# Kernel tuning notes

Measured on AMD Instinct MI355X. Metric: run time of the kernel, lower is better.

## Reference

```python
import jax, jax.numpy as jnp
import numpy as np

B, S, HID = 2, 2048, 2816
NH, NKV, HD = 16, 8, 256
WINDOW = 1024
EPS = 1e-6
ROPE_THETA = 10000.0


def _rope_cos_sin(batch, seq, dim, theta):
    inv_freq = 1.0 / (theta ** (np.arange(0, dim, 2, dtype=np.float32) / dim))  # [dim/2]
    pos = np.arange(seq, dtype=np.float32)
    freqs = np.outer(pos, inv_freq)                 # [S, dim/2]
    emb = np.concatenate([freqs, freqs], axis=-1)   # [S, dim]
    cos = np.broadcast_to(np.cos(emb), (batch, seq, dim))
    sin = np.broadcast_to(np.sin(emb), (batch, seq, dim))
    return jnp.asarray(cos), jnp.asarray(sin)


def setup_inputs() -> dict:
    key = jax.random.key(0)
    ks = jax.random.split(key, 6)
    hidden_states = jax.random.normal(ks[0], (B, S, HID), dtype=jnp.float32)
    sc = 0.02
    Wq = jax.random.normal(ks[1], (NH * HD, HID), dtype=jnp.float32) * sc
    Wk = jax.random.normal(ks[2], (NKV * HD, HID), dtype=jnp.float32) * sc
    Wv = jax.random.normal(ks[3], (NKV * HD, HID), dtype=jnp.float32) * sc
    Wo = jax.random.normal(ks[4], (HID, NH * HD), dtype=jnp.float32) * sc
    q_norm_w = jnp.ones((HD,), dtype=jnp.float32) + 0.1 * jax.random.normal(ks[5], (HD,), dtype=jnp.float32)
    k_norm_w = jnp.ones((HD,), dtype=jnp.float32)
    cos, sin = _rope_cos_sin(B, S, HD, ROPE_THETA)
    return {"hidden_states": hidden_states, "Wq": Wq, "Wk": Wk, "Wv": Wv,
            "Wo": Wo, "q_norm_w": q_norm_w, "k_norm_w": k_norm_w,
            "cos": cos, "sin": sin}


def _rmsnorm(x, w):
    # HF Gemma4: effective weight, no +1 offset
    var = jnp.mean(jnp.square(x), axis=-1, keepdims=True)
    return x * jax.lax.rsqrt(var + EPS) * w


def _rotate_half(x):
    h = x.shape[-1] // 2
    return jnp.concatenate([-x[..., h:], x[..., :h]], axis=-1)


def reference(hidden_states, Wq, Wk, Wv, Wo, q_norm_w, k_norm_w, cos, sin):
    b, s, _ = hidden_states.shape
    q = (hidden_states @ Wq.T).reshape(b, s, NH, HD)
    k = (hidden_states @ Wk.T).reshape(b, s, NKV, HD)
    v = (hidden_states @ Wv.T).reshape(b, s, NKV, HD)
    q = _rmsnorm(q, q_norm_w)
    k = _rmsnorm(k, k_norm_w)
    v = _rmsnorm(v, jnp.ones((HD,), dtype=v.dtype))  # v_norm has no scale
    # RoPE with explicit cos/sin, unsqueeze at head dim (2)
    c = cos[:, :, None, :]
    sn = sin[:, :, None, :]
    q = q * c + _rotate_half(q) * sn
    k = k * c + _rotate_half(k) * sn
    # GQA: repeat kv heads to match query heads
    rep = NH // NKV
    k = jnp.repeat(k, rep, axis=2)  # [b,s,NH,HD]
    v = jnp.repeat(v, rep, axis=2)
    # scale=1.0 per torch_attention call (no 1/sqrt(d))
    scores = jnp.einsum('bqhd,bkhd->bhqk', q, k)
    i = jnp.arange(s)[:, None]
    j = jnp.arange(s)[None, :]
    mask = (j <= i) & (i - j < WINDOW)  # causal + sliding window
    scores = jnp.where(mask[None, None], scores, jnp.finfo(scores.dtype).min)
    attn = jax.nn.softmax(scores, axis=-1)
    out = jnp.einsum('bhqk,bkhd->bqhd', attn, v)  # [b,s,NH,HD]
    return out.reshape(b, s, NH * HD) @ Wo.T
```

## Files before the change

### kernel.cpp

```cpp
#include <hip/hip_runtime.h>
#include <math.h>

typedef unsigned short u16;
typedef __attribute__((ext_vector_type(8))) short short8;
typedef __attribute__((ext_vector_type(8))) _Float16 half8;
typedef __attribute__((ext_vector_type(4))) float floatx4;

#define NH 16
#define NKV 8
#define HD 256
#define SEQ 2048
#define BATCH 2
#define QD (NH * HD)
#define KVD (NKV * HD)
#define TOKS (BATCH * SEQ)
#define WINDOW 1024

__device__ __forceinline__ u16 f2h(float f) {
    _Float16 h = (_Float16)f;
    return __builtin_bit_cast(u16, h);
}
__device__ __forceinline__ float h2f(u16 u) {
    return (float)__builtin_bit_cast(_Float16, u);
}

__device__ __forceinline__ void gload16(const u16* g, u16* l) {
    __builtin_amdgcn_global_load_lds(
        (const __attribute__((address_space(1))) unsigned int*)g,
        (__attribute__((address_space(3))) unsigned int*)l,
        16, 0, 0);
}

__global__ __launch_bounds__(256) void f32_to_f16(const float* __restrict__ in,
                                                  u16* __restrict__ out, int n8) {
    const int i = blockIdx.x * 256 + threadIdx.x;
    if (i >= n8) return;
    const float4 a = *((const float4*)in + 2 * (size_t)i);
    const float4 b = *((const float4*)in + 2 * (size_t)i + 1);
    short8 r;
    r[0] = (short)f2h(a.x); r[1] = (short)f2h(a.y);
    r[2] = (short)f2h(a.z); r[3] = (short)f2h(a.w);
    r[4] = (short)f2h(b.x); r[5] = (short)f2h(b.y);
    r[6] = (short)f2h(b.z); r[7] = (short)f2h(b.w);
    *((short8*)out + i) = r;
}

template<bool OUTF32, bool OUTT>
__global__ __launch_bounds__(256) void gemm_lds(const u16* __restrict__ A,
                                                const u16* __restrict__ B,
                                                void* __restrict__ Cp,
                                                int M, int N, int K) {
    __shared__ u16 As[128 * 32];
    __shared__ u16 Bs[128 * 32];

    const int tid = threadIdx.x;
    const int wave = tid >> 6, lane = tid & 63;
    const int quad = lane >> 4, l16 = lane & 15;
    const int bm = blockIdx.y * 128, bn = blockIdx.x * 128;
    const int wm = (wave >> 1) * 64, wn = (wave & 1) * 64;

    const int srow = wave * 32 + (lane >> 2);
    const int scol = (lane & 3) * 8;
    const u16* ga0 = A + (size_t)(bm + srow) * K + scol;
    const u16* ga1 = ga0 + (size_t)16 * K;
    const u16* gb0 = B + (size_t)(bn + srow) * K + scol;
    const u16* gb1 = gb0 + (size_t)16 * K;
    u16* lA0 = &As[wave * 1024];
    u16* lA1 = &As[wave * 1024 + 512];
    u16* lB0 = &Bs[wave * 1024];
    u16* lB1 = &Bs[wave * 1024 + 512];

    floatx4 acc[4][4];
#pragma unroll
    for (int i = 0; i < 4; ++i)
#pragma unroll
        for (int j = 0; j < 4; ++j) acc[i][j] = (floatx4){0.f, 0.f, 0.f, 0.f};

    const int kTiles = K >> 5;
    for (int kt = 0; kt < kTiles; ++kt) {
        __syncthreads();
        gload16(ga0, lA0);
        gload16(ga1, lA1);
        gload16(gb0, lB0);
        gload16(gb1, lB1);
        ga0 += 32; ga1 += 32; gb0 += 32; gb1 += 32;
        __syncthreads();

        half8 af[4], bfr[4];
#pragma unroll
        for (int i = 0; i < 4; ++i)
            af[i] = *(const half8*)(&As[(wm + i * 16 + l16) * 32 + quad * 8]);
#pragma unroll
        for (int j = 0; j < 4; ++j)
            bfr[j] = *(const half8*)(&Bs[(wn + j * 16 + l16) * 32 + quad * 8]);
#pragma unroll
        for (int i = 0; i < 4; ++i)
#pragma unroll
            for (int j = 0; j < 4; ++j)
                acc[i][j] = __builtin_amdgcn_mfma_f32_16x16x32_f16(af[i], bfr[j], acc[i][j], 0, 0, 0);
    }

#pragma unroll
    for (int i = 0; i < 4; ++i) {
#pragma unroll
        for (int j = 0; j < 4; ++j) {
            const int row0 = bm + wm + i * 16 + quad * 4;
            const int col = bn + wn + j * 16 + l16;
#pragma unroll
            for (int r = 0; r < 4; ++r) {
                if constexpr (OUTT)
                    ((u16*)Cp)[(size_t)col * M + row0 + r] = f2h(acc[i][j][r]);
                else if constexpr (OUTF32)
                    ((float*)Cp)[(size_t)(row0 + r) * N + col] = acc[i][j][r];
                else
                    ((u16*)Cp)[(size_t)(row0 + r) * N + col] = f2h(acc[i][j][r]);
            }
        }
    }
}

__global__ __launch_bounds__(256) void norm_rope_kernel(
        u16* __restrict__ Q, u16* __restrict__ K,
        const float* __restrict__ qw, const float* __restrict__ kw,
        const float* __restrict__ cosp, const float* __restrict__ sinp) {
    const int w = blockIdx.x * 4 + (threadIdx.x >> 6);
    const int lane = threadIdx.x & 63;
    const int row = w >> 5;
    const int sub = w & 31;
    if (sub >= 24) return;

    u16* ptr;
    const float* wt;
    if (sub < 16) { ptr = Q + (size_t)row * QD + sub * HD;         wt = qw; }
    else          { ptr = K + (size_t)row * KVD + (sub - 16) * HD; wt = kw; }

    const int d = lane * 4;
    uint2 raw = *(const uint2*)(ptr + d);
    float x[4];
    x[0] = h2f((u16)(raw.x & 0xffffu));
    x[1] = h2f((u16)(raw.x >> 16));
    x[2] = h2f((u16)(raw.y & 0xffffu));
    x[3] = h2f((u16)(raw.y >> 16));

    float ss = x[0] * x[0] + x[1] * x[1] + x[2] * x[2] + x[3] * x[3];
#pragma unroll
    for (int m = 1; m < 64; m <<= 1) ss += __shfl_xor(ss, m, 64);
    const float sc = rsqrtf(ss * (1.0f / 256.0f) + 1e-6f);

    float nrm[4];
#pragma unroll
    for (int i = 0; i < 4; ++i) nrm[i] = x[i] * sc * wt[d + i];

    const size_t cbase = (size_t)row * HD + d;
    const float sgn = (lane < 32) ? -1.0f : 1.0f;
    float out[4];
#pragma unroll
    for (int i = 0; i < 4; ++i) {
        float pn = __shfl_xor(nrm[i], 32, 64);
        float c = cosp[cbase + i];
        float s = sinp[cbase + i];
        out[i] = nrm[i] * c + sgn * pn * s;
    }

    uint2 o;
    o.x = (unsigned int)f2h(out[0]) | ((unsigned int)f2h(out[1]) << 16);
    o.y = (unsigned int)f2h(out[2]) | ((unsigned int)f2h(out[3]) << 16);
    *(uint2*)(ptr + d) = o;
}

__global__ __launch_bounds__(256) void vnorm_kernel(u16* __restrict__ Vt) {
    const int tok = blockIdx.x * 256 + threadIdx.x;
    const int kvh = blockIdx.y;
    u16* p = Vt + (size_t)kvh * HD * TOKS + tok;
    float ss = 0.f;
#pragma unroll 4
    for (int d = 0; d < HD; ++d) {
        float v = h2f(p[(size_t)d * TOKS]);
        ss += v * v;
    }
    const float sc = rsqrtf(ss * (1.0f / 256.0f) + 1e-6f);
#pragma unroll 4
    for (int d = 0; d < HD; ++d) {
        const size_t idx = (size_t)d * TOKS;
        p[idx] = f2h(h2f(p[idx]) * sc);
    }
}

#define QBLK 64
#define KVBLK 64

__global__ __launch_bounds__(256, 2) void attn_mfma(
        const u16* __restrict__ Q, const u16* __restrict__ K,
        const u16* __restrict__ Vt, u16* __restrict__ O) {
    __shared__ u16 Ks[64 * 264];
    __shared__ u16 Vs[256 * 72];
    __shared__ u16 Ps[4][16 * 72];

    const int tid = threadIdx.x;
    const int wave = tid >> 6, lane = tid & 63;
    const int quad = lane >> 4, l16 = lane & 15;
    const int q0 = blockIdx.x * QBLK;
    const int h = blockIdx.y, b = blockIdx.z;
    const int kvh = h >> 1;

    half8 qf[8];
    {
        const u16* qp = Q + (size_t)(b * SEQ + q0 + wave * 16 + l16) * QD + h * HD + quad * 8;
#pragma unroll
        for (int s = 0; s < 8; ++s) qf[s] = *(const half8*)(qp + s * 32);
    }

    float mrow[4], lrow[4];
#pragma unroll
    for (int r = 0; r < 4; ++r) { mrow[r] = -1e30f; lrow[r] = 0.f; }
    floatx4 o[16];
#pragma unroll
    for (int n = 0; n < 16; ++n) o[n] = (floatx4){0.f, 0.f, 0.f, 0.f};

    int lo = q0 - (WINDOW - 1);
    const int t0 = (lo > 0 ? lo : 0) >> 6;
    const int tq = q0 >> 6;

    for (int t = t0; t <= tq; ++t) {
        const int k0 = t * KVBLK;
        __syncthreads();
        {
            const int r = tid >> 5, c = (tid & 31) * 8;
            const u16* kp = K + (size_t)(b * SEQ + k0 + r) * KVD + kvh * HD + c;
#pragma unroll
            for (int p = 0; p < 8; ++p)
                *(short8*)(&Ks[(r + p * 8) * 264 + c]) = *(const short8*)(kp + (size_t)(p * 8) * KVD);
        }
        {
            const int r = tid >> 3, c = (tid & 7) * 8;
            const u16* vp = Vt + (size_t)(kvh * HD + r) * TOKS + b * SEQ + k0 + c;
#pragma unroll
            for (int p = 0; p < 8; ++p)
                *(short8*)(&Vs[(r + p * 32) * 72 + c]) = *(const short8*)(vp + (size_t)(p * 32) * TOKS);
        }
        __syncthreads();

        floatx4 sf[4];
#pragma unroll
        for (int j = 0; j < 4; ++j) sf[j] = (floatx4){0.f, 0.f, 0.f, 0.f};
#pragma unroll
        for (int s = 0; s < 8; ++s) {
#pragma unroll
            for (int j = 0; j < 4; ++j) {
                half8 bf = *(const half8*)(&Ks[(j * 16 + l16) * 264 + s * 32 + quad * 8]);
                sf[j] = __builtin_amdgcn_mfma_f32_16x16x32_f16(qf[s], bf, sf[j], 0, 0, 0);
            }
        }

        const bool needMask = (t == tq) || ((q0 + QBLK - 1) - k0 >= WINDOW);
        if (needMask) {
#pragma unroll
            for (int j = 0; j < 4; ++j) {
                const int kg = k0 + j * 16 + l16;
#pragma unroll
                for (int r = 0; r < 4; ++r) {
                    const int qg = q0 + wave * 16 + quad * 4 + r;
                    if (kg > qg || qg - kg >= WINDOW) sf[j][r] = -1e30f;
                }
            }
        }

#pragma unroll
        for (int r = 0; r < 4; ++r) {
            float mx = fmaxf(fmaxf(sf[0][r], sf[1][r]), fmaxf(sf[2][r], sf[3][r]));
            mx = fmaxf(mx, __shfl_xor(mx, 1, 64));
            mx = fmaxf(mx, __shfl_xor(mx, 2, 64));
            mx = fmaxf(mx, __shfl_xor(mx, 4, 64));
            mx = fmaxf(mx, __shfl_xor(mx, 8, 64));
            const float mnew = fmaxf(mrow[r], mx);
            const float rescale = __expf(mrow[r] - mnew);
            mrow[r] = mnew;
            float pv[4], ssum = 0.f;
#pragma unroll
            for (int j = 0; j < 4; ++j) {
                pv[j] = __expf(sf[j][r] - mnew);
                ssum += pv[j];
            }
            ssum += __shfl_xor(ssum, 1, 64);
            ssum += __shfl_xor(ssum, 2, 64);
            ssum += __shfl_xor(ssum, 4, 64);
            ssum += __shfl_xor(ssum, 8, 64);
            lrow[r] = lrow[r] * rescale + ssum;
#pragma unroll
            for (int n = 0; n < 16; ++n) o[n][r] *= rescale;
#pragma unroll
            for (int j = 0; j < 4; ++j)
                Ps[wave][(quad * 4 + r) * 72 + j * 16 + l16] = f2h(pv[j]);
        }

#pragma unroll
        for (int s2 = 0; s2 < 2; ++s2) {
            half8 pa = *(const half8*)(&Ps[wave][l16 * 72 + s2 * 32 + quad * 8]);
#pragma unroll
            for (int n = 0; n < 16; ++n) {
                half8 vb = *(const half8*)(&Vs[(n * 16 + l16) * 72 + s2 * 32 + quad * 8]);
                o[n] = __builtin_amdgcn_mfma_f32_16x16x32_f16(pa, vb, o[n], 0, 0, 0);
            }
        }
    }

#pragma unroll
    for (int r = 0; r < 4; ++r) {
        const float inv = 1.0f / lrow[r];
        const size_t base = (size_t)(b * SEQ + q0 + wave * 16 + quad * 4 + r) * QD + h * HD + l16;
#pragma unroll
        for (int n = 0; n < 16; ++n)
            O[base + n * 16] = f2h(o[n][r] * inv);
    }
}

extern "C" void kernel_launch(void* const* d_in, const int* in_sizes, int n_in,
                              void* d_out, int out_size, void* d_ws, size_t ws_size,
                              hipStream_t stream) {
    const float* X    = (const float*)d_in[0];
    const float* Wq   = (const float*)d_in[1];
    const float* Wk   = (const float*)d_in[2];
    const float* Wv   = (const float*)d_in[3];
    const float* Wo   = (const float*)d_in[4];
    const float* qw   = (const float*)d_in[5];
    const float* kw   = (const float*)d_in[6];
    const float* cosp = (const float*)d_in[7];
    const float* sinp = (const float*)d_in[8];

    char* ws = (char*)d_ws;
    u16* Qb  = (u16*)(ws);
    u16* Kb  = (u16*)(ws + (size_t)33554432);
    u16* Vt  = (u16*)(ws + (size_t)50331648);
    u16* Ob  = (u16*)(ws + (size_t)67108864);
    u16* Wkh = (u16*)(ws + (size_t)67108864);
    u16* Wvh = (u16*)(ws + (size_t)78643200);
    u16* Woh = (u16*)(ws);

    u16* Xh  = (u16*)d_out;
    u16* Wqh = (u16*)d_out + (size_t)11534336;

    const dim3 blk(256);
    f32_to_f16<<<dim3(5632), blk, 0, stream>>>(X,  Xh,  11534336 / 8);
    f32_to_f16<<<dim3(5632), blk, 0, stream>>>(Wq, Wqh, 11534336 / 8);
    gemm_lds<false, false><<<dim3(4096 / 128, 4096 / 128), blk, 0, stream>>>(Xh, Wqh, Qb, 4096, 4096, 2816);
    f32_to_f16<<<dim3(2816), blk, 0, stream>>>(Wk, Wkh, 5767168 / 8);
    gemm_lds<false, false><<<dim3(2048 / 128, 4096 / 128), blk, 0, stream>>>(Xh, Wkh, Kb, 4096, 2048, 2816);
    f32_to_f16<<<dim3(2816), blk, 0, stream>>>(Wv, Wvh, 5767168 / 8);
    gemm_lds<false, true ><<<dim3(2048 / 128, 4096 / 128), blk, 0, stream>>>(Xh, Wvh, Vt, 4096, 2048, 2816);
    norm_rope_kernel<<<dim3((BATCH * SEQ * 32) / 4), blk, 0, stream>>>(Qb, Kb, qw, kw, cosp, sinp);
    vnorm_kernel<<<dim3(TOKS / 256, NKV), blk, 0, stream>>>(Vt);
    attn_mfma<<<dim3(SEQ / QBLK, NH, BATCH), blk, 0, stream>>>(Qb, Kb, Vt, Ob);
    f32_to_f16<<<dim3(5632), blk, 0, stream>>>(Wo, Woh, 11534336 / 8);
    gemm_lds<true, false><<<dim3(2816 / 128, 4096 / 128), blk, 0, stream>>>(Ob, Woh, d_out, 4096, 2816, 4096);
}
```

Measured before the change: 858.4 us.

## Fuse QKV projections into one GEMM and swizzle attention LDS with async loads

The three Q/K/V projection GEMMs become one launch over a concatenated fp16 weight matrix. Each output tile is routed to Q, K or transposed V storage depending on its column block. The attention kernel now loads its K/V tiles with direct global-to-LDS 16-byte loads into unpadded, XOR-swizzled shared buffers, replacing register-staged copies into padded arrays. It also raises wave priority around the MFMA sections. The intent is fewer launches, better GEMM occupancy, less LDS footprint and fewer bank conflicts, at the cost of more complex addressing and fp16 buffers placed in the output region.

Result: faster. 833.3 us (-2.9%).

```diff
diff --git a/kernel.cpp b/kernel.cpp
--- a/kernel.cpp
+++ b/kernel.cpp
@@ -45,61 +45,58 @@
     *((short8*)out + i) = r;
 }
 
-template<bool OUTF32, bool OUTT>
+#define GEMM_PRE()                                                            \
+    __shared__ u16 As[128 * 32];                                              \
+    __shared__ u16 Bs[128 * 32];                                              \
+    const int tid = threadIdx.x;                                              \
+    const int wave = tid >> 6, lane = tid & 63;                               \
+    const int quad = lane >> 4, l16 = lane & 15;                              \
+    const int bm = blockIdx.y * 128, bn = blockIdx.x * 128;                   \
+    const int wm = (wave >> 1) * 64, wn = (wave & 1) * 64;                    \
+    const int srow = wave * 32 + (lane >> 2);                                 \
+    const int scol = (lane & 3) * 8;                                          \
+    const u16* ga0 = A + (size_t)(bm + srow) * K + scol;                      \
+    const u16* ga1 = ga0 + (size_t)16 * K;                                    \
+    const u16* gb0 = B + (size_t)(bn + srow) * K + scol;                      \
+    const u16* gb1 = gb0 + (size_t)16 * K;                                    \
+    u16* lA0 = &As[wave * 1024];                                              \
+    u16* lA1 = &As[wave * 1024 + 512];                                        \
+    u16* lB0 = &Bs[wave * 1024];                                              \
+    u16* lB1 = &Bs[wave * 1024 + 512];                                        \
+    floatx4 acc[4][4];                                                        \
+    _Pragma("unroll")                                                         \
+    for (int i = 0; i < 4; ++i)                                               \
+        _Pragma("unroll")                                                     \
+        for (int j = 0; j < 4; ++j) acc[i][j] = (floatx4){0.f, 0.f, 0.f, 0.f};\
+    const int kTiles = K >> 5;                                                \
+    for (int kt = 0; kt < kTiles; ++kt) {                                     \
+        __syncthreads();                                                      \
+        gload16(ga0, lA0);                                                    \
+        gload16(ga1, lA1);                                                    \
+        gload16(gb0, lB0);                                                    \
+        gload16(gb1, lB1);                                                    \
+        ga0 += 32; ga1 += 32; gb0 += 32; gb1 += 32;                           \
+        __syncthreads();                                                      \
+        half8 af[4], bfr[4];                                                  \
+        _Pragma("unroll")                                                     \
+        for (int i = 0; i < 4; ++i)                                           \
+            af[i] = *(const half8*)(&As[(wm + i * 16 + l16) * 32 + quad * 8]);\
+        _Pragma("unroll")                                                     \
+        for (int j = 0; j < 4; ++j)                                           \
+            bfr[j] = *(const half8*)(&Bs[(wn + j * 16 + l16) * 32 + quad * 8]);\
+        _Pragma("unroll")                                                     \
+        for (int i = 0; i < 4; ++i)                                           \
+            _Pragma("unroll")                                                 \
+            for (int j = 0; j < 4; ++j)                                       \
+                acc[i][j] = __builtin_amdgcn_mfma_f32_16x16x32_f16(af[i], bfr[j], acc[i][j], 0, 0, 0); \
+    }
+
+template<bool OUTF32>
 __global__ __launch_bounds__(256) void gemm_lds(const u16* __restrict__ A,
                                                 const u16* __restrict__ B,
                                                 void* __restrict__ Cp,
                                                 int M, int N, int K) {
-    __shared__ u16 As[128 * 32];
-    __shared__ u16 Bs[128 * 32];
-
-    const int tid = threadIdx.x;
-    const int wave = tid >> 6, lane = tid & 63;
-    const int quad = lane >> 4, l16 = lane & 15;
-    const int bm = blockIdx.y * 128, bn = blockIdx.x * 128;
-    const int wm = (wave >> 1) * 64, wn = (wave & 1) * 64;
-
-    const int srow = wave * 32 + (lane >> 2);
-    const int scol = (lane & 3) * 8;
-    const u16* ga0 = A + (size_t)(bm + srow) * K + scol;
-    const u16* ga1 = ga0 + (size_t)16 * K;
-    const u16* gb0 = B + (size_t)(bn + srow) * K + scol;
-    const u16* gb1 = gb0 + (size_t)16 * K;
-    u16* lA0 = &As[wave * 1024];
-    u16* lA1 = &As[wave * 1024 + 512];
-    u16* lB0 = &Bs[wave * 1024];
-    u16* lB1 = &Bs[wave * 1024 + 512];
-
-    floatx4 acc[4][4];
-#pragma unroll
-    for (int i = 0; i < 4; ++i)
-#pragma unroll
-        for (int j = 0; j < 4; ++j) acc[i][j] = (floatx4){0.f, 0.f, 0.f, 0.f};
-
-    const int kTiles = K >> 5;
-    for (int kt = 0; kt < kTiles; ++kt) {
-        __syncthreads();
-        gload16(ga0, lA0);
-        gload16(ga1, lA1);
-        gload16(gb0, lB0);
-        gload16(gb1, lB1);
-        ga0 += 32; ga1 += 32; gb0 += 32; gb1 += 32;
-        __syncthreads();
-
-        half8 af[4], bfr[4];
-#pragma unroll
-        for (int i = 0; i < 4; ++i)
-            af[i] = *(const half8*)(&As[(wm + i * 16 + l16) * 32 + quad * 8]);
-#pragma unroll
-        for (int j = 0; j < 4; ++j)
-            bfr[j] = *(const half8*)(&Bs[(wn + j * 16 + l16) * 32 + quad * 8]);
-#pragma unroll
-        for (int i = 0; i < 4; ++i)
-#pragma unroll
-            for (int j = 0; j < 4; ++j)
-                acc[i][j] = __builtin_amdgcn_mfma_f32_16x16x32_f16(af[i], bfr[j], acc[i][j], 0, 0, 0);
-    }
-
+    GEMM_PRE()
 #pragma unroll
     for (int i = 0; i < 4; ++i) {
 #pragma unroll
@@ -108,12 +105,37 @@
             const int col = bn + wn + j * 16 + l16;
 #pragma unroll
             for (int r = 0; r < 4; ++r) {
-                if constexpr (OUTT)
-                    ((u16*)Cp)[(size_t)col * M + row0 + r] = f2h(acc[i][j][r]);
-                else if constexpr (OUTF32)
+                if constexpr (OUTF32)
                     ((float*)Cp)[(size_t)(row0 + r) * N + col] = acc[i][j][r];
                 else
                     ((u16*)Cp)[(size_t)(row0 + r) * N + col] = f2h(acc[i][j][r]);
+            }
+        }
+    }
+}
+
+__global__ __launch_bounds__(256) void gemm_qkv(const u16* __restrict__ A,
+                                                const u16* __restrict__ B,
+                                                u16* __restrict__ Qb,
+                                                u16* __restrict__ Kb,
+                                                u16* __restrict__ Vt,
+                                                int M, int N, int K) {
+    GEMM_PRE()
+#pragma unroll
+    for (int i = 0; i < 4; ++i) {
+#pragma unroll
+        for (int j = 0; j < 4; ++j) {
+            const int row0 = bm + wm + i * 16 + quad * 4;
+            const int col = bn + wn + j * 16 + l16;
+#pragma unroll
+            for (int r = 0; r < 4; ++r) {
+                const u16 hv = f2h(acc[i][j][r]);
+                if (bn < 4096)
+                    Qb[(size_t)(row0 + r) * QD + col] = hv;
+                else if (bn < 6144)
+                    Kb[(size_t)(row0 + r) * KVD + (col - 4096)] = hv;
+                else
+                    Vt[(size_t)(col - 6144) * TOKS + row0 + r] = hv;
             }
         }
     }
@@ -192,8 +214,8 @@
 __global__ __launch_bounds__(256, 2) void attn_mfma(
         const u16* __restrict__ Q, const u16* __restrict__ K,
         const u16* __restrict__ Vt, u16* __restrict__ O) {
-    __shared__ u16 Ks[64 * 264];
-    __shared__ u16 Vs[256 * 72];
+    __shared__ u16 Ks[64 * 256];
+    __shared__ u16 Vs[256 * 64];
     __shared__ u16 Ps[4][16 * 72];
 
     const int tid = threadIdx.x;
@@ -221,36 +243,44 @@
     const int t0 = (lo > 0 ? lo : 0) >> 6;
     const int tq = q0 >> 6;
 
+    const int kr2 = wave * 2 + (lane >> 5);
+    const int kcb = (lane & 31) * 16;
+    const int vr8 = wave * 8 + (lane >> 3);
+    const int vcb = (lane & 7) * 16;
+
     for (int t = t0; t <= tq; ++t) {
         const int k0 = t * KVBLK;
         __syncthreads();
-        {
-            const int r = tid >> 5, c = (tid & 31) * 8;
-            const u16* kp = K + (size_t)(b * SEQ + k0 + r) * KVD + kvh * HD + c;
-#pragma unroll
-            for (int p = 0; p < 8; ++p)
-                *(short8*)(&Ks[(r + p * 8) * 264 + c]) = *(const short8*)(kp + (size_t)(p * 8) * KVD);
-        }
-        {
-            const int r = tid >> 3, c = (tid & 7) * 8;
-            const u16* vp = Vt + (size_t)(kvh * HD + r) * TOKS + b * SEQ + k0 + c;
-#pragma unroll
-            for (int p = 0; p < 8; ++p)
-                *(short8*)(&Vs[(r + p * 32) * 72 + c]) = *(const short8*)(vp + (size_t)(p * 32) * TOKS);
+#pragma unroll
+        for (int p = 0; p < 8; ++p) {
+            const int row = p * 8 + kr2;
+            const int scb = kcb ^ ((row & 7) << 4);
+            const u16* g = K + (size_t)(b * SEQ + k0 + row) * KVD + kvh * HD + (scb >> 1);
+            gload16(g, &Ks[p * 2048 + wave * 512]);
+        }
+#pragma unroll
+        for (int p = 0; p < 8; ++p) {
+            const int row = p * 32 + vr8;
+            const int scb = vcb ^ ((row & 7) << 4);
+            const u16* g = Vt + (size_t)(kvh * HD + row) * TOKS + b * SEQ + k0 + (scb >> 1);
+            gload16(g, &Vs[p * 2048 + wave * 512]);
         }
         __syncthreads();
 
         floatx4 sf[4];
 #pragma unroll
         for (int j = 0; j < 4; ++j) sf[j] = (floatx4){0.f, 0.f, 0.f, 0.f};
+        __builtin_amdgcn_s_setprio(1);
 #pragma unroll
         for (int s = 0; s < 8; ++s) {
 #pragma unroll
             for (int j = 0; j < 4; ++j) {
-                half8 bf = *(const half8*)(&Ks[(j * 16 + l16) * 264 + s * 32 + quad * 8]);
+                half8 bf = *(const half8*)(&Ks[(j * 16 + l16) * 256 +
+                                               ((s * 32 + quad * 8) ^ ((l16 & 7) << 3))]);
                 sf[j] = __builtin_amdgcn_mfma_f32_16x16x32_f16(qf[s], bf, sf[j], 0, 0, 0);
             }
         }
+        __builtin_amdgcn_s_setprio(0);
 
         const bool needMask = (t == tq) || ((q0 + QBLK - 1) - k0 >= WINDOW);
         if (needMask) {
@@ -293,15 +323,18 @@
                 Ps[wave][(quad * 4 + r) * 72 + j * 16 + l16] = f2h(pv[j]);
         }
 
+        __builtin_amdgcn_s_setprio(1);
 #pragma unroll
         for (int s2 = 0; s2 < 2; ++s2) {
             half8 pa = *(const half8*)(&Ps[wave][l16 * 72 + s2 * 32 + quad * 8]);
 #pragma unroll
             for (int n = 0; n < 16; ++n) {
-                half8 vb = *(const half8*)(&Vs[(n * 16 + l16) * 72 + s2 * 32 + quad * 8]);
+                half8 vb = *(const half8*)(&Vs[(n * 16 + l16) * 64 +
+                                               ((s2 * 32 + quad * 8) ^ ((l16 & 7) << 3))]);
                 o[n] = __builtin_amdgcn_mfma_f32_16x16x32_f16(pa, vb, o[n], 0, 0, 0);
             }
         }
+        __builtin_amdgcn_s_setprio(0);
     }
 
 #pragma unroll
@@ -331,25 +364,21 @@
     u16* Qb  = (u16*)(ws);
     u16* Kb  = (u16*)(ws + (size_t)33554432);
     u16* Vt  = (u16*)(ws + (size_t)50331648);
+    u16* Xh  = (u16*)(ws + (size_t)67108864);
     u16* Ob  = (u16*)(ws + (size_t)67108864);
-    u16* Wkh = (u16*)(ws + (size_t)67108864);
-    u16* Wvh = (u16*)(ws + (size_t)78643200);
     u16* Woh = (u16*)(ws);
 
-    u16* Xh  = (u16*)d_out;
-    u16* Wqh = (u16*)d_out + (size_t)11534336;
+    u16* Wqkv = (u16*)d_out;
 
     const dim3 blk(256);
-    f32_to_f16<<<dim3(5632), blk, 0, stream>>>(X,  Xh,  11534336 / 8);
-    f32_to_f16<<<dim3(5632), blk, 0, stream>>>(Wq, Wqh, 11534336 / 8);
-    gemm_lds<false, false><<<dim3(4096 / 128, 4096 / 128), blk, 0, stream>>>(Xh, Wqh, Qb, 4096, 4096, 2816);
-    f32_to_f16<<<dim3(2816), blk, 0, stream>>>(Wk, Wkh, 5767168 / 8);
-    gemm_lds<false, false><<<dim3(2048 / 128, 4096 / 128), blk, 0, stream>>>(Xh, Wkh, Kb, 4096, 2048, 2816);
-    f32_to_f16<<<dim3(2816), blk, 0, stream>>>(Wv, Wvh, 5767168 / 8);
-    gemm_lds<false, true ><<<dim3(2048 / 128, 4096 / 128), blk, 0, stream>>>(Xh, Wvh, Vt, 4096, 2048, 2816);
+    f32_to_f16<<<dim3(5632), blk, 0, stream>>>(X,  Xh, 11534336 / 8);
+    f32_to_f16<<<dim3(5632), blk, 0, stream>>>(Wq, Wqkv, 11534336 / 8);
+    f32_to_f16<<<dim3(2816), blk, 0, stream>>>(Wk, Wqkv + (size_t)4096 * 2816, 5767168 / 8);
+    f32_to_f16<<<dim3(2816), blk, 0, stream>>>(Wv, Wqkv + (size_t)6144 * 2816, 5767168 / 8);
+    gemm_qkv<<<dim3(8192 / 128, 4096 / 128), blk, 0, stream>>>(Xh, Wqkv, Qb, Kb, Vt, 4096, 8192, 2816);
     norm_rope_kernel<<<dim3((BATCH * SEQ * 32) / 4), blk, 0, stream>>>(Qb, Kb, qw, kw, cosp, sinp);
     vnorm_kernel<<<dim3(TOKS / 256, NKV), blk, 0, stream>>>(Vt);
     attn_mfma<<<dim3(SEQ / QBLK, NH, BATCH), blk, 0, stream>>>(Qb, Kb, Vt, Ob);
     f32_to_f16<<<dim3(5632), blk, 0, stream>>>(Wo, Woh, 11534336 / 8);
-    gemm_lds<true, false><<<dim3(2816 / 128, 4096 / 128), blk, 0, stream>>>(Ob, Woh, d_out, 4096, 2816, 4096);
-}
+    gemm_lds<true><<<dim3(2816 / 128, 4096 / 128), blk, 0, stream>>>(Ob, Woh, d_out, 4096, 2816, 4096);
+}
```

## Fuse QKV projections into one 256x256 tiled GEMM and swizzle attention LDS

Applied to the files above, without the earlier changes.

Q, K and V weights are converted into one concatenated fp16 buffer, and a new 512-thread GEMM with 256x256 tiles, double-buffered direct-to-LDS loads and XOR-swizzled LDS produces Q, K and transposed V in a single launch. The output projection GEMM gets an XCD-aware workgroup remap. The attention kernel replaces padded LDS copies with swizzled direct global-to-LDS loads and raises wave priority around its MFMA sections. The aim is fewer launches, more reuse of X across the projections, and fewer LDS bank conflicts. The cost is much higher register and LDS use per block, with a risk of spills.

Result: faster. 778.9 us (-9.3%).

```diff
diff --git a/kernel.cpp b/kernel.cpp
--- a/kernel.cpp
+++ b/kernel.cpp
@@ -45,7 +45,108 @@
     *((short8*)out + i) = r;
 }
 
-template<bool OUTF32, bool OUTT>
+#define QKV_K 2816
+#define QKV_NT (QKV_K / 64)
+
+__global__ __launch_bounds__(512, 2) void gemm256_qkv(
+        const u16* __restrict__ A, const u16* __restrict__ B,
+        u16* __restrict__ Qb, u16* __restrict__ Kb, u16* __restrict__ Vt) {
+    __shared__ u16 As[2 * 16384];
+    __shared__ u16 Bs[2 * 16384];
+
+    const int tid = threadIdx.x;
+    const int wave = tid >> 6, lane = tid & 63;
+    const int quad = lane >> 4, l16 = lane & 15;
+    const int wr = wave >> 2, wc = wave & 3;
+
+    const int wg0 = (int)blockIdx.x;
+    const int wg = (wg0 & 7) * 64 + (wg0 >> 3);
+    const int bm = (wg >> 5) * 256;
+    const int bn = (wg & 31) * 256;
+    const int K = QKV_K;
+
+    const int srow = wave * 8 + (lane >> 3);
+    const int scu = ((lane & 7) ^ (lane >> 3)) << 3;
+    const u16* gA = A + (size_t)(bm + srow) * K + scu;
+    const u16* gB = B + (size_t)(bn + srow) * K + scu;
+
+    floatx4 acc[8][4];
+#pragma unroll
+    for (int i = 0; i < 8; ++i)
+#pragma unroll
+        for (int j = 0; j < 4; ++j) acc[i][j] = (floatx4){0.f, 0.f, 0.f, 0.f};
+
+#define STG(tt, bb)                                                           \
+    {                                                                         \
+        const int k0_ = (tt) * 64;                                            \
+        _Pragma("unroll")                                                     \
+        for (int r2 = 0; r2 < 4; ++r2) {                                      \
+            gload16(gA + k0_ + (size_t)(r2 * 64) * K,                         \
+                    &As[(bb) * 16384 + r2 * 4096 + wave * 512]);              \
+            gload16(gB + k0_ + (size_t)(r2 * 64) * K,                         \
+                    &Bs[(bb) * 16384 + r2 * 4096 + wave * 512]);              \
+        }                                                                     \
+    }
+
+    STG(0, 0);
+
+    for (int t = 0; t < QKV_NT; ++t) {
+        const int cb = t & 1;
+        if (t + 1 < QKV_NT) {
+            STG(t + 1, cb ^ 1);
+            asm volatile("s_waitcnt vmcnt(8)" ::: "memory");
+        } else {
+            asm volatile("s_waitcnt vmcnt(0)" ::: "memory");
+        }
+        __builtin_amdgcn_sched_barrier(0);
+        __builtin_amdgcn_s_barrier();
+        __builtin_amdgcn_sched_barrier(0);
+
+#pragma unroll
+        for (int kk = 0; kk < 2; ++kk) {
+            half8 bq[4], aq[8];
+#pragma unroll
+            for (int j = 0; j < 4; ++j)
+                bq[j] = *(const half8*)(&Bs[cb * 16384 + (wc * 64 + j * 16 + l16) * 64 +
+                                            ((kk * 32 + quad * 8) ^ ((l16 & 7) << 3))]);
+#pragma unroll
+            for (int i = 0; i < 8; ++i)
+                aq[i] = *(const half8*)(&As[cb * 16384 + (wr * 128 + i * 16 + l16) * 64 +
+                                            ((kk * 32 + quad * 8) ^ ((l16 & 7) << 3))]);
+#pragma unroll
+            for (int i = 0; i < 8; ++i)
+#pragma unroll
+                for (int j = 0; j < 4; ++j)
+                    acc[i][j] = __builtin_amdgcn_mfma_f32_16x16x32_f16(aq[i], bq[j], acc[i][j], 0, 0, 0);
+        }
+
+        __builtin_amdgcn_sched_barrier(0);
+        __builtin_amdgcn_s_barrier();
+        __builtin_amdgcn_sched_barrier(0);
+    }
+#undef STG
+
+#pragma unroll
+    for (int i = 0; i < 8; ++i) {
+#pragma unroll
+        for (int j = 0; j < 4; ++j) {
+            const int row0 = bm + wr * 128 + i * 16 + quad * 4;
+            const int col = bn + wc * 64 + j * 16 + l16;
+#pragma unroll
+            for (int r = 0; r < 4; ++r) {
+                const u16 hv = f2h(acc[i][j][r]);
+                if (bn < 4096)
+                    Qb[(size_t)(row0 + r) * QD + col] = hv;
+                else if (bn < 6144)
+                    Kb[(size_t)(row0 + r) * KVD + (col - 4096)] = hv;
+                else
+                    Vt[(size_t)(col - 6144) * TOKS + row0 + r] = hv;
+            }
+        }
+    }
+}
+
+template<bool OUTF32>
 __global__ __launch_bounds__(256) void gemm_lds(const u16* __restrict__ A,
                                                 const u16* __restrict__ B,
                                                 void* __restrict__ Cp,
@@ -56,7 +157,11 @@
     const int tid = threadIdx.x;
     const int wave = tid >> 6, lane = tid & 63;
     const int quad = lane >> 4, l16 = lane & 15;
-    const int bm = blockIdx.y * 128, bn = blockIdx.x * 128;
+
+    int wg = blockIdx.y * gridDim.x + blockIdx.x;
+    const int nwg = gridDim.x * gridDim.y;
+    if ((nwg & 7) == 0) wg = (wg & 7) * (nwg >> 3) + (wg >> 3);
+    const int bm = (wg / gridDim.x) * 128, bn = (wg % gridDim.x) * 128;
     const int wm = (wave >> 1) * 64, wn = (wave & 1) * 64;
 
     const int srow = wave * 32 + (lane >> 2);
@@ -108,9 +213,7 @@
             const int col = bn + wn + j * 16 + l16;
 #pragma unroll
             for (int r = 0; r < 4; ++r) {
-                if constexpr (OUTT)
-                    ((u16*)Cp)[(size_t)col * M + row0 + r] = f2h(acc[i][j][r]);
-                else if constexpr (OUTF32)
+                if constexpr (OUTF32)
                     ((float*)Cp)[(size_t)(row0 + r) * N + col] = acc[i][j][r];
                 else
                     ((u16*)Cp)[(size_t)(row0 + r) * N + col] = f2h(acc[i][j][r]);
@@ -192,8 +295,8 @@
 __global__ __launch_bounds__(256, 2) void attn_mfma(
         const u16* __restrict__ Q, const u16* __restrict__ K,
         const u16* __restrict__ Vt, u16* __restrict__ O) {
-    __shared__ u16 Ks[64 * 264];
-    __shared__ u16 Vs[256 * 72];
+    __shared__ u16 Ks[64 * 256];
+    __shared__ u16 Vs[256 * 64];
     __shared__ u16 Ps[4][16 * 72];
 
     const int tid = threadIdx.x;
@@ -221,36 +324,44 @@
     const int t0 = (lo > 0 ? lo : 0) >> 6;
     const int tq = q0 >> 6;
 
+    const int kr2 = wave * 2 + (lane >> 5);
+    const int kcb = (lane & 31) * 16;
+    const int vr8 = wave * 8 + (lane >> 3);
+    const int vcb = (lane & 7) * 16;
+
     for (int t = t0; t <= tq; ++t) {
         const int k0 = t * KVBLK;
         __syncthreads();
-        {
-            const int r = tid >> 5, c = (tid & 31) * 8;
-            const u16* kp = K + (size_t)(b * SEQ + k0 + r) * KVD + kvh * HD + c;
-#pragma unroll
-            for (int p = 0; p < 8; ++p)
-                *(short8*)(&Ks[(r + p * 8) * 264 + c]) = *(const short8*)(kp + (size_t)(p * 8) * KVD);
-        }
-        {
-            const int r = tid >> 3, c = (tid & 7) * 8;
-            const u16* vp = Vt + (size_t)(kvh * HD + r) * TOKS + b * SEQ + k0 + c;
-#pragma unroll
-            for (int p = 0; p < 8; ++p)
-                *(short8*)(&Vs[(r + p * 32) * 72 + c]) = *(const short8*)(vp + (size_t)(p * 32) * TOKS);
+#pragma unroll
+        for (int p = 0; p < 8; ++p) {
+            const int row = p * 8 + kr2;
+            const int scb = kcb ^ ((row & 7) << 4);
+            const u16* g = K + (size_t)(b * SEQ + k0 + row) * KVD + kvh * HD + (scb >> 1);
+            gload16(g, &Ks[p * 2048 + wave * 512]);
+        }
+#pragma unroll
+        for (int p = 0; p < 8; ++p) {
+            const int row = p * 32 + vr8;
+            const int scb = vcb ^ ((row & 7) << 4);
+            const u16* g = Vt + (size_t)(kvh * HD + row) * TOKS + b * SEQ + k0 + (scb >> 1);
+            gload16(g, &Vs[p * 2048 + wave * 512]);
         }
         __syncthreads();
 
         floatx4 sf[4];
 #pragma unroll
         for (int j = 0; j < 4; ++j) sf[j] = (floatx4){0.f, 0.f, 0.f, 0.f};
+        __builtin_amdgcn_s_setprio(1);
 #pragma unroll
         for (int s = 0; s < 8; ++s) {
 #pragma unroll
             for (int j = 0; j < 4; ++j) {
-                half8 bf = *(const half8*)(&Ks[(j * 16 + l16) * 264 + s * 32 + quad * 8]);
+                half8 bf = *(const half8*)(&Ks[(j * 16 + l16) * 256 +
+                                               ((s * 32 + quad * 8) ^ ((l16 & 7) << 3))]);
                 sf[j] = __builtin_amdgcn_mfma_f32_16x16x32_f16(qf[s], bf, sf[j], 0, 0, 0);
             }
         }
+        __builtin_amdgcn_s_setprio(0);
 
         const bool needMask = (t == tq) || ((q0 + QBLK - 1) - k0 >= WINDOW);
         if (needMask) {
@@ -293,15 +404,18 @@
                 Ps[wave][(quad * 4 + r) * 72 + j * 16 + l16] = f2h(pv[j]);
         }
 
+        __builtin_amdgcn_s_setprio(1);
 #pragma unroll
         for (int s2 = 0; s2 < 2; ++s2) {
             half8 pa = *(const half8*)(&Ps[wave][l16 * 72 + s2 * 32 + quad * 8]);
 #pragma unroll
             for (int n = 0; n < 16; ++n) {
-                half8 vb = *(const half8*)(&Vs[(n * 16 + l16) * 72 + s2 * 32 + quad * 8]);
+                half8 vb = *(const half8*)(&Vs[(n * 16 + l16) * 64 +
+                                               ((s2 * 32 + quad * 8) ^ ((l16 & 7) << 3))]);
                 o[n] = __builtin_amdgcn_mfma_f32_16x16x32_f16(pa, vb, o[n], 0, 0, 0);
             }
         }
+        __builtin_amdgcn_s_setprio(0);
     }
 
 #pragma unroll
@@ -331,25 +445,21 @@
     u16* Qb  = (u16*)(ws);
     u16* Kb  = (u16*)(ws + (size_t)33554432);
     u16* Vt  = (u16*)(ws + (size_t)50331648);
+    u16* Xh  = (u16*)(ws + (size_t)67108864);
     u16* Ob  = (u16*)(ws + (size_t)67108864);
-    u16* Wkh = (u16*)(ws + (size_t)67108864);
-    u16* Wvh = (u16*)(ws + (size_t)78643200);
     u16* Woh = (u16*)(ws);
 
-    u16* Xh  = (u16*)d_out;
-    u16* Wqh = (u16*)d_out + (size_t)11534336;
+    u16* Wqkv = (u16*)d_out;
 
     const dim3 blk(256);
-    f32_to_f16<<<dim3(5632), blk, 0, stream>>>(X,  Xh,  11534336 / 8);
-    f32_to_f16<<<dim3(5632), blk, 0, stream>>>(Wq, Wqh, 11534336 / 8);
-    gemm_lds<false, false><<<dim3(4096 / 128, 4096 / 128), blk, 0, stream>>>(Xh, Wqh, Qb, 4096, 4096, 2816);
-    f32_to_f16<<<dim3(2816), blk, 0, stream>>>(Wk, Wkh, 5767168 / 8);
-    gemm_lds<false, false><<<dim3(2048 / 128, 4096 / 128), blk, 0, stream>>>(Xh, Wkh, Kb, 4096, 2048, 2816);
-    f32_to_f16<<<dim3(2816), blk, 0, stream>>>(Wv, Wvh, 5767168 / 8);
-    gemm_lds<false, true ><<<dim3(2048 / 128, 4096 / 128), blk, 0, stream>>>(Xh, Wvh, Vt, 4096, 2048, 2816);
+    f32_to_f16<<<dim3(5632), blk, 0, stream>>>(X,  Xh, 11534336 / 8);
+    f32_to_f16<<<dim3(5632), blk, 0, stream>>>(Wq, Wqkv, 11534336 / 8);
+    f32_to_f16<<<dim3(2816), blk, 0, stream>>>(Wk, Wqkv + (size_t)4096 * 2816, 5767168 / 8);
+    f32_to_f16<<<dim3(2816), blk, 0, stream>>>(Wv, Wqkv + (size_t)6144 * 2816, 5767168 / 8);
+    gemm256_qkv<<<dim3(512), dim3(512), 0, stream>>>(Xh, Wqkv, Qb, Kb, Vt);
     norm_rope_kernel<<<dim3((BATCH * SEQ * 32) / 4), blk, 0, stream>>>(Qb, Kb, qw, kw, cosp, sinp);
     vnorm_kernel<<<dim3(TOKS / 256, NKV), blk, 0, stream>>>(Vt);
     attn_mfma<<<dim3(SEQ / QBLK, NH, BATCH), blk, 0, stream>>>(Qb, Kb, Vt, Ob);
     f32_to_f16<<<dim3(5632), blk, 0, stream>>>(Wo, Woh, 11534336 / 8);
-    gemm_lds<true, false><<<dim3(2816 / 128, 4096 / 128), blk, 0, stream>>>(Ob, Woh, d_out, 4096, 2816, 4096);
-}
+    gemm_lds<true><<<dim3(2816 / 128, 4096 / 128), blk, 0, stream>>>(Ob, Woh, d_out, 4096, 2816, 4096);
+}
```
